# Kernel tuning notes

Hardware: AMD Instinct MI355X
Metric: run time of the kernel (lower is better)

## Reference

```python
import jax, jax.numpy as jnp
import numpy as np

F_DIM = 1024
D = F_DIM // 2          # trunk width (divisor=2)
T = 1024                # contextlen
B = 32
PI = 256
VF = 256
N_HEADS = 4
EPS = 1e-5


def _posenc(seq_len, d):
    pos = jnp.arange(seq_len, dtype=jnp.float32)[:, None]
    div = jnp.exp(jnp.arange(0, d, 2, dtype=jnp.float32) * (-np.log(10000.0) / d))
    pe = jnp.zeros((seq_len, d), dtype=jnp.float32)
    pe = pe.at[:, 0::2].set(jnp.sin(pos * div))
    pe = pe.at[:, 1::2].set(jnp.cos(pos * div))
    return pe


def _ln(x, g, b):
    mu = x.mean(-1, keepdims=True)
    var = ((x - mu) ** 2).mean(-1, keepdims=True)
    return (x - mu) / jnp.sqrt(var + EPS) * g + b


def setup_inputs() -> dict:
    key = jax.random.key(0)
    ks = iter(jax.random.split(key, 40))
    w = lambda shape: jax.random.normal(next(ks), shape, dtype=jnp.float32) * 0.02
    inp = {
        "features": jax.random.normal(next(ks), (B, T, F_DIM), dtype=jnp.float32),
        "enc_w1": w((F_DIM, D)), "enc_b1": jnp.zeros((D,), jnp.float32),
        "enc_w2": w((D, D)),     "enc_b2": jnp.zeros((D,), jnp.float32),
        "qkv_w": w((D, 3 * D)),  "qkv_b": jnp.zeros((3 * D,), jnp.float32),
        "lam": jnp.float32(0.8),
        "out_w": w((D, D)),      "out_b": jnp.zeros((D,), jnp.float32),
        "ln1_g": jnp.ones((D,), jnp.float32), "ln1_b": jnp.zeros((D,), jnp.float32),
        "ffn_w1": w((D, F_DIM)), "ffn_b1": jnp.zeros((F_DIM,), jnp.float32),
        "ffn_w2": w((F_DIM, D)), "ffn_b2": jnp.zeros((D,), jnp.float32),
        "ln2_g": jnp.ones((D,), jnp.float32), "ln2_b": jnp.zeros((D,), jnp.float32),
        "act_w1": w((D, F_DIM)),       "act_b1": jnp.zeros((F_DIM,), jnp.float32),
        "act_w2": w((F_DIM, 2 * F_DIM)), "act_b2": jnp.zeros((2 * F_DIM,), jnp.float32),
        "act_w3": w((2 * F_DIM, PI)),  "act_b3": jnp.zeros((PI,), jnp.float32),
        "cr_w1": w((D, F_DIM)),        "cr_b1": jnp.zeros((F_DIM,), jnp.float32),
        "cr_w2": w((F_DIM, 2 * F_DIM)), "cr_b2": jnp.zeros((2 * F_DIM,), jnp.float32),
        "cr_w3": w((2 * F_DIM, VF)),   "cr_b3": jnp.zeros((VF,), jnp.float32),
    }
    return inp


def reference(features, enc_w1, enc_b1, enc_w2, enc_b2, qkv_w, qkv_b, lam,
              out_w, out_b, ln1_g, ln1_b, ffn_w1, ffn_b1, ffn_w2, ffn_b2,
              ln2_g, ln2_b, act_w1, act_b1, act_w2, act_b2, act_w3, act_b3,
              cr_w1, cr_b1, cr_w2, cr_b2, cr_w3, cr_b3):
    b, t, f = features.shape
    # encoder MLP: feature_dim -> d -> d with ReLU
    y = jax.nn.relu(features @ enc_w1 + enc_b1)
    y = jax.nn.relu(y @ enc_w2 + enc_b2)            # (B,T,D)
    d = y.shape[-1]
    y = y + _posenc(t, d)
    # differential dual-softmax attention (no head split; head_dim only scales)
    qkv = y @ qkv_w + qkv_b
    q, k, v = jnp.split(qkv, 3, axis=-1)
    q1, q2 = jnp.split(q, 2, axis=-1)
    k1, k2 = jnp.split(k, 2, axis=-1)
    scale = 1.0 / np.sqrt(d // N_HEADS)
    a1 = jax.nn.softmax(jnp.einsum('btc,bsc->bts', q1, k1) * scale, axis=-1)
    a2 = jax.nn.softmax(jnp.einsum('btc,bsc->bts', q2, k2) * scale, axis=-1)
    diff = a1 - lam * a2
    attn = jnp.einsum('bts,bsd->btd', diff, v)      # (B,T,D)
    # faithful to torch: transpose(0,1).contiguous().view(B,-1,D)
    attn = jnp.swapaxes(attn, 0, 1).reshape(b, t, d)
    attn = attn @ out_w + out_b
    y = _ln(y + attn, ln1_g, ln1_b)
    z = jax.nn.relu(y @ ffn_w1 + ffn_b1) @ ffn_w2 + ffn_b2
    y = _ln(y + z, ln2_g, ln2_b)                     # (B,T,D)
    # actor / critic heads, then take last timestep
    a = jax.nn.relu(y @ act_w1 + act_b1)
    a = jax.nn.relu(a @ act_w2 + act_b2)
    a = a @ act_w3 + act_b3
    c = jax.nn.relu(y @ cr_w1 + cr_b1)
    c = jax.nn.relu(c @ cr_w2 + cr_b2)
    c = c @ cr_w3 + cr_b3
    return (a[:, -1, :], c[:, -1, :])
```

## Files before the change

### kernel.cpp

```cpp
#include <hip/hip_runtime.h>
#include <hip/hip_bf16.h>
#include <math.h>

#define TDIM 1024
#define FDIM 1024
#define DDIM 512

typedef __attribute__((ext_vector_type(8))) short bf16x8;
typedef __attribute__((ext_vector_type(8))) ushort u16x8;
typedef __attribute__((ext_vector_type(4))) float f32x4;

__device__ __forceinline__ float posenc_val(int t, int c) {
    int j = c >> 1;
    float dv = expf(-9.210340371976184f * (float)(2 * j) * (1.0f / 512.0f));
    float arg = (float)t * dv;
    return (c & 1) ? cosf(arg) : sinf(arg);
}

__device__ __forceinline__ ushort f2bf(float f) {
    __hip_bfloat16 h = __float2bfloat16(f);
    return *reinterpret_cast<ushort*>(&h);
}

template<int BK>
__device__ __forceinline__ void g32_body(
    const float* X, long lda,
    const float* Pin, int KCx, const float* xbias, int xrelu,
    const float* W, long ldb,
    float* Pout, int N, int K,
    int bx, int by, float* lds)
{
    float (*Xs)[BK + 4] = (float (*)[BK + 4])lds;
    float (*Ws)[64]     = (float (*)[64])(lds + 32 * (BK + 4));
    const int tid = threadIdx.x;
    const int n0 = bx * 64, k0 = by * BK;

    {
        const int m  = tid >> 3;
        const int ks = (tid & 7) * (BK / 8);
        if (Pin) {
            #pragma unroll
            for (int j = 0; j < BK / 32; ++j) {
                float4 a = make_float4(0.f, 0.f, 0.f, 0.f);
                for (int c = 0; c < KCx; ++c) {
                    float4 v = *(const float4*)(Pin + (size_t)(c * 32 + m) * K + k0 + ks + j * 4);
                    a.x += v.x; a.y += v.y; a.z += v.z; a.w += v.w;
                }
                if (xbias) {
                    float4 bv = *(const float4*)(xbias + k0 + ks + j * 4);
                    a.x += bv.x; a.y += bv.y; a.z += bv.z; a.w += bv.w;
                }
                if (xrelu) {
                    a.x = fmaxf(a.x, 0.f); a.y = fmaxf(a.y, 0.f);
                    a.z = fmaxf(a.z, 0.f); a.w = fmaxf(a.w, 0.f);
                }
                *(float4*)&Xs[m][ks + j * 4] = a;
            }
        } else {
            const float* src = X + (size_t)m * lda + k0 + ks;
            #pragma unroll
            for (int j = 0; j < BK / 32; ++j)
                *(float4*)&Xs[m][ks + j * 4] = *(const float4*)(src + j * 4);
        }
    }
    #pragma unroll
    for (int it = 0; it < BK / 16; ++it) {
        int e4  = it * 256 + tid;
        int row = e4 >> 4;
        int c4  = e4 & 15;
        *(float4*)&Ws[row][c4 * 4] = *(const float4*)(W + (size_t)(k0 + row) * ldb + n0 + c4 * 4);
    }
    __syncthreads();

    const int tx = tid & 31;
    const int ty = tid >> 5;
    float acc[4][2] = {};
    #pragma unroll 8
    for (int k = 0; k < BK; k += 4) {
        float4 xv[4];
        #pragma unroll
        for (int i = 0; i < 4; ++i) xv[i] = *(const float4*)&Xs[ty * 4 + i][k];
        #pragma unroll
        for (int j = 0; j < 4; ++j) {
            float2 w = *(const float2*)&Ws[k + j][tx * 2];
            #pragma unroll
            for (int i = 0; i < 4; ++i) {
                float x = ((const float*)&xv[i])[j];
                acc[i][0] = fmaf(x, w.x, acc[i][0]);
                acc[i][1] = fmaf(x, w.y, acc[i][1]);
            }
        }
    }
    float* dst = Pout + (size_t)by * 32 * N;
    #pragma unroll
    for (int i = 0; i < 4; ++i)
        *(float2*)(dst + (size_t)(ty * 4 + i) * N + n0 + tx * 2) = make_float2(acc[i][0], acc[i][1]);
}

template<int BK>
__global__ __launch_bounds__(256) void g32k(
    const float* X0, const float* X1, long lda,
    const float* Pin0, const float* Pin1, int KCx,
    const float* xb0, const float* xb1, int xrelu,
    const float* W0, const float* W1, long ldb,
    float* Pout, int N, int K)
{
    __shared__ __align__(16) float lds[32 * (BK + 4) + BK * 64];
    const int z = blockIdx.z;
    g32_body<BK>(z ? X1 : X0, lda, z ? Pin1 : Pin0, KCx, z ? xb1 : xb0, xrelu,
                 z ? W1 : W0, ldb,
                 Pout + (size_t)z * gridDim.y * 32 * N,
                 N, K, blockIdx.x, blockIdx.y, lds);
}

__device__ __forceinline__ void convT_body(const float* W, int ldw, int col0,
                                           ushort* Wt, int K, int bx, int by, float* lds)
{
    float (*t)[33] = (float (*)[33])lds;
    const int k0 = by * 32, n0 = bx * 32;
    const int x = threadIdx.x & 31, y = threadIdx.x >> 5;
    #pragma unroll
    for (int yy = y; yy < 32; yy += 8)
        t[yy][x] = W[(size_t)(k0 + yy) * ldw + col0 + n0 + x];
    __syncthreads();
    #pragma unroll
    for (int yy = y; yy < 32; yy += 8)
        Wt[(size_t)(n0 + yy) * K + k0 + x] = f2bf(t[x][yy]);
}

__device__ __forceinline__ void mfma_body(
    const void* Aptr, int af32, long lda,
    const ushort* Bt, const float* bias,
    float* C, int ldc, ushort* Cbf, int ldcb,
    int K, int relu, int addpe,
    int bx, int by, char* smem)
{
    ushort* Al = (ushort*)smem;
    ushort* Bl = Al + 64 * 64;
    const int tid = threadIdx.x;
    const int m0 = by * 64;
    const int n0 = bx * 64;
    const int lane = tid & 63;
    const int wv = tid >> 6;
    const int wr = wv >> 1, wc = wv & 1;
    const int fr = lane & 15, g = lane >> 4;

    f32x4 acc[2][2] = {};

    const int r0 = tid >> 3;
    const int c0 = tid & 7;

    for (int k0 = 0; k0 < K; k0 += 64) {
        #pragma unroll
        for (int it = 0; it < 2; ++it) {
            int r = r0 + it * 32;
            if (af32) {
                const float* Af = (const float*)Aptr;
                const float* s = Af + (size_t)(m0 + r) * lda + k0 + c0 * 8;
                float4 u = *(const float4*)s;
                float4 v = *(const float4*)(s + 4);
                u16x8 pv;
                pv[0] = f2bf(u.x); pv[1] = f2bf(u.y); pv[2] = f2bf(u.z); pv[3] = f2bf(u.w);
                pv[4] = f2bf(v.x); pv[5] = f2bf(v.y); pv[6] = f2bf(v.z); pv[7] = f2bf(v.w);
                *(u16x8*)((char*)Al + r * 128 + ((c0 ^ (r & 7)) << 4)) = pv;
            } else {
                const ushort* Au = (const ushort*)Aptr;
                uint4 va = *(const uint4*)(Au + (size_t)(m0 + r) * lda + k0 + c0 * 8);
                *(uint4*)((char*)Al + r * 128 + ((c0 ^ (r & 7)) << 4)) = va;
            }
            uint4 vb = *(const uint4*)(Bt + (size_t)(n0 + r) * K + k0 + c0 * 8);
            *(uint4*)((char*)Bl + r * 128 + ((c0 ^ (r & 7)) << 4)) = vb;
        }
        __syncthreads();
        #pragma unroll
        for (int h = 0; h < 2; ++h) {
            bf16x8 af[2], bff[2];
            #pragma unroll
            for (int i = 0; i < 2; ++i) {
                int row = wr * 32 + i * 16 + fr;
                af[i] = *(const bf16x8*)((const char*)Al + row * 128 + (((h * 4 + g) ^ (row & 7)) << 4));
                int col = wc * 32 + i * 16 + fr;
                bff[i] = *(const bf16x8*)((const char*)Bl + col * 128 + (((h * 4 + g) ^ (col & 7)) << 4));
            }
            #pragma unroll
            for (int i = 0; i < 2; ++i)
                #pragma unroll
                for (int j = 0; j < 2; ++j)
                    acc[i][j] = __builtin_amdgcn_mfma_f32_16x16x32_bf16(af[i], bff[j], acc[i][j], 0, 0, 0);
        }
        __syncthreads();
    }

    #pragma unroll
    for (int j = 0; j < 2; ++j) {
        int n = n0 + wc * 32 + j * 16 + fr;
        float bv = bias ? bias[n] : 0.f;
        #pragma unroll
        for (int i = 0; i < 2; ++i) {
            #pragma unroll
            for (int q = 0; q < 4; ++q) {
                int m = m0 + wr * 32 + i * 16 + g * 4 + q;
                float v = acc[i][j][q] + bv;
                if (relu) v = fmaxf(v, 0.f);
                if (addpe) v += posenc_val(m, n);
                if (C)   C[(size_t)m * ldc + n] = v;
                if (Cbf) Cbf[(size_t)m * ldcb + n] = f2bf(v);
            }
        }
    }
}

__global__ __launch_bounds__(256) void mfma_k(
    const void* A, int af32, long lda, const ushort* Bt, const float* bias,
    float* C, int ldc, ushort* Cbf, int ldcb, int K, int relu, int pe)
{
    __shared__ __align__(16) char smem[16384];
    mfma_body(A, af32, lda, Bt, bias, C, ldc, Cbf, ldcb, K, relu, pe,
              blockIdx.x, blockIdx.y, smem);
}

__global__ __launch_bounds__(256) void prep_k(
    const float* features, const float* enc_w1, const float* qkv_w, const float* enc_w2,
    ushort* w1T, ushort* w2T, ushort* qkvT, float* P_enc1)
{
    __shared__ __align__(16) float lds[6272];
    int t = blockIdx.x;
    if (t < 128) {
        g32_body<64>(features + (size_t)1023 * FDIM, (long)TDIM * FDIM,
                     nullptr, 0, nullptr, 0,
                     enc_w1, DDIM, P_enc1, 512, 1024, t & 7, t >> 3, lds);
    } else if (t < 640) {
        int u = t - 128;
        convT_body(enc_w1, 512, 0, w1T, 1024, u & 15, u >> 4, lds);
    } else if (t < 896) {
        int u = t - 640;
        convT_body(enc_w2, 512, 0, w2T, 512, u & 15, u >> 4, lds);
    } else {
        int u = t - 896;
        convT_body(qkv_w, 1536, 0, qkvT, 512, u % 48, u / 48, lds);
    }
}

__global__ __launch_bounds__(256) void stage2_k(
    const float* features31, const ushort* w1T, const float* enc_b1, ushort* H1bf,
    const float* P_enc1, const float* enc_w2, float* P_enc2)
{
    __shared__ __align__(16) char smem[25600];
    int t = blockIdx.x;
    if (t < 128) {
        mfma_body(features31, 1, 1024, w1T, enc_b1, nullptr, 0, H1bf, 512,
                  1024, 1, 0, t & 7, t >> 3, smem);
    } else {
        int u = t - 128;
        g32_body<64>(nullptr, 0, P_enc1, 16, enc_b1, 1,
                     enc_w2, 512, P_enc2, 512, 512, u & 7, u >> 3, (float*)smem);
    }
}

__device__ void scores_body(const float* QKV, float* Psc, int bxs, int byc, char* smem)
{
    float (*Kt)[132] = (float (*)[132])smem;
    float (*Qt)[133] = (float (*)[133])(smem + 64 * 132 * 4);
    const int tid = threadIdx.x;
    const int s0 = bxs * 64;
    const int k0 = byc * 128;

    #pragma unroll
    for (int it = 0; it < 8; ++it) {
        int e4 = it * 256 + tid;
        int r  = e4 >> 5;
        int c4 = e4 & 31;
        float4 v = *(const float4*)(QKV + (size_t)(s0 + r) * 1536 + 512 + k0 + c4 * 4);
        *(float4*)&Kt[r][c4 * 4] = v;
    }
    #pragma unroll
    for (int it = 0; it < 4; ++it) {
        int e4 = it * 256 + tid;
        int r  = e4 >> 5;
        int c4 = e4 & 31;
        float4 v = *(const float4*)(QKV + (size_t)(32 * r + 31) * 1536 + k0 + c4 * 4);
        Qt[r][c4 * 4 + 0] = v.x;
        Qt[r][c4 * 4 + 1] = v.y;
        Qt[r][c4 * 4 + 2] = v.z;
        Qt[r][c4 * 4 + 3] = v.w;
    }
    __syncthreads();

    const int i  = tid & 31;
    const int sg = tid >> 5;
    float acc[8] = {};
    for (int k = 0; k < 128; ++k) {
        float q = Qt[i][k];
        #pragma unroll
        for (int j = 0; j < 8; ++j)
            acc[j] = fmaf(Kt[sg * 8 + j][k], q, acc[j]);
    }
    float* dst = Psc + (size_t)byc * 1024 * 32;
    #pragma unroll
    for (int j = 0; j < 8; ++j)
        dst[(size_t)(s0 + sg * 8 + j) * 32 + i] = acc[j];
}

__global__ __launch_bounds__(256) void stage5_k(
    const float* QKV, float* Psc,
    const float* P_enc2, const float* enc_b2, float* ylast)
{
    __shared__ __align__(16) char smem[50816];
    int t = blockIdx.x;
    if (t < 64) {
        scores_body(QKV, Psc, t & 15, t >> 4, smem);
    } else {
        int blk = t - 64;
        for (int idx = threadIdx.x; idx < 4 * 512; idx += 256) {
            int r = idx >> 9, c = idx & 511;
            int m = blk * 4 + r;
            float s = enc_b2[c];
            for (int cc = 0; cc < 8; ++cc) s += P_enc2[(size_t)(cc * 32 + m) * 512 + c];
            s = fmaxf(s, 0.f) + posenc_val(1023, c);
            ylast[m * 512 + c] = s;
        }
    }
}

__global__ __launch_bounds__(256) void softmax_diff(
    const float* __restrict__ Psc, const float* __restrict__ lam_p, float* __restrict__ D)
{
    __shared__ float sc1[TDIM];
    __shared__ float sc2[TDIM];
    __shared__ float red[256];
    const int i = blockIdx.x;
    const int tid = threadIdx.x;
    const float scale = 0.08838834764831845f;
    for (int s = tid; s < TDIM; s += 256) {
        float a = Psc[(size_t)(0 * 1024 + s) * 32 + i] + Psc[(size_t)(1 * 1024 + s) * 32 + i];
        float b = Psc[(size_t)(2 * 1024 + s) * 32 + i] + Psc[(size_t)(3 * 1024 + s) * 32 + i];
        sc1[s] = a * scale;
        sc2[s] = b * scale;
    }
    __syncthreads();
    float m1 = -INFINITY, m2 = -INFINITY;
    for (int s = tid; s < TDIM; s += 256) { m1 = fmaxf(m1, sc1[s]); m2 = fmaxf(m2, sc2[s]); }
    red[tid] = m1; __syncthreads();
    for (int o = 128; o > 0; o >>= 1) { if (tid < o) red[tid] = fmaxf(red[tid], red[tid + o]); __syncthreads(); }
    m1 = red[0]; __syncthreads();
    red[tid] = m2; __syncthreads();
    for (int o = 128; o > 0; o >>= 1) { if (tid < o) red[tid] = fmaxf(red[tid], red[tid + o]); __syncthreads(); }
    m2 = red[0]; __syncthreads();
    float t1 = 0.f, t2 = 0.f;
    for (int s = tid; s < TDIM; s += 256) { t1 += expf(sc1[s] - m1); t2 += expf(sc2[s] - m2); }
    red[tid] = t1; __syncthreads();
    for (int o = 128; o > 0; o >>= 1) { if (tid < o) red[tid] += red[tid + o]; __syncthreads(); }
    t1 = red[0]; __syncthreads();
    red[tid] = t2; __syncthreads();
    for (int o = 128; o > 0; o >>= 1) { if (tid < o) red[tid] += red[tid + o]; __syncthreads(); }
    t2 = red[0]; __syncthreads();
    const float inv1 = 1.f / t1, inv2 = 1.f / t2;
    const float lam = *lam_p;
    for (int s = tid; s < TDIM; s += 256)
        D[(size_t)i * TDIM + s] = expf(sc1[s] - m1) * inv1 - lam * expf(sc2[s] - m2) * inv2;
}

__global__ __launch_bounds__(256) void ln_red(
    const float* __restrict__ Pin, int KC, const float* __restrict__ bias,
    const float* __restrict__ R, const float* __restrict__ g, const float* __restrict__ b,
    float* __restrict__ Y)
{
    __shared__ float red[256];
    const int m = blockIdx.x;
    const int tid = threadIdx.x;
    float v0 = bias ? bias[tid] : 0.f;
    float v1 = bias ? bias[tid + 256] : 0.f;
    for (int c = 0; c < KC; ++c) {
        v0 += Pin[(size_t)(c * 32 + m) * 512 + tid];
        v1 += Pin[(size_t)(c * 32 + m) * 512 + tid + 256];
    }
    v0 += R[m * 512 + tid];
    v1 += R[m * 512 + tid + 256];
    red[tid] = v0 + v1; __syncthreads();
    for (int o = 128; o > 0; o >>= 1) { if (tid < o) red[tid] += red[tid + o]; __syncthreads(); }
    const float mu = red[0] * (1.0f / 512.0f);
    __syncthreads();
    float d0 = v0 - mu, d1 = v1 - mu;
    red[tid] = d0 * d0 + d1 * d1; __syncthreads();
    for (int o = 128; o > 0; o >>= 1) { if (tid < o) red[tid] += red[tid + o]; __syncthreads(); }
    const float var = red[0] * (1.0f / 512.0f);
    const float inv = 1.0f / sqrtf(var + 1e-5f);
    Y[m * 512 + tid]       = d0 * inv * g[tid]       + b[tid];
    Y[m * 512 + 256 + tid] = d1 * inv * g[256 + tid] + b[256 + tid];
}

__global__ __launch_bounds__(256) void fin_out(
    const float* __restrict__ P, const float* __restrict__ b0, const float* __restrict__ b1,
    float* __restrict__ out)
{
    const int m = blockIdx.x;
    const int z = blockIdx.y;
    const int n = threadIdx.x;
    const float* bias = z ? b1 : b0;
    const float* Pz = P + (size_t)z * 16 * 32 * 256;
    float s = bias[n];
    for (int c = 0; c < 16; ++c) s += Pz[(size_t)(c * 32 + m) * 256 + n];
    out[z * 8192 + m * 256 + n] = s;
}

extern "C" void kernel_launch(void* const* d_in, const int* in_sizes, int n_in,
                              void* d_out, int out_size, void* d_ws, size_t ws_size,
                              hipStream_t stream)
{
    const float* features = (const float*)d_in[0];
    const float* enc_w1 = (const float*)d_in[1];
    const float* enc_b1 = (const float*)d_in[2];
    const float* enc_w2 = (const float*)d_in[3];
    const float* enc_b2 = (const float*)d_in[4];
    const float* qkv_w  = (const float*)d_in[5];
    const float* qkv_b  = (const float*)d_in[6];
    const float* lam    = (const float*)d_in[7];
    const float* out_w  = (const float*)d_in[8];
    const float* out_b  = (const float*)d_in[9];
    const float* ln1_g  = (const float*)d_in[10];
    const float* ln1_b  = (const float*)d_in[11];
    const float* ffn_w1 = (const float*)d_in[12];
    const float* ffn_b1 = (const float*)d_in[13];
    const float* ffn_w2 = (const float*)d_in[14];
    const float* ffn_b2 = (const float*)d_in[15];
    const float* ln2_g  = (const float*)d_in[16];
    const float* ln2_b  = (const float*)d_in[17];
    const float* act_w1 = (const float*)d_in[18];
    const float* act_b1 = (const float*)d_in[19];
    const float* act_w2 = (const float*)d_in[20];
    const float* act_b2 = (const float*)d_in[21];
    const float* act_w3 = (const float*)d_in[22];
    const float* act_b3 = (const float*)d_in[23];
    const float* cr_w1  = (const float*)d_in[24];
    const float* cr_b1  = (const float*)d_in[25];
    const float* cr_w2  = (const float*)d_in[26];
    const float* cr_b2  = (const float*)d_in[27];
    const float* cr_w3  = (const float*)d_in[28];
    const float* cr_b3  = (const float*)d_in[29];
    float* out = (float*)d_out;

    char* base = (char*)d_ws;
    ushort* w1T    = (ushort*)(base + 0x000000);
    ushort* w2T    = (ushort*)(base + 0x100000);
    ushort* qkvT   = (ushort*)(base + 0x180000);
    ushort* H1bf   = (ushort*)(base + 0x300000);
    ushort* Y31bf  = (ushort*)(base + 0x400000);
    float*  QKV    = (float*)(base + 0x500000);
    float*  Psc    = (float*)(base + 0xB00000);
    float*  Dbuf   = (float*)(base + 0xB80000);
    float*  ylast  = (float*)(base + 0xBA0000);
    float*  y1     = (float*)(base + 0xBB0000);
    float*  y2     = (float*)(base + 0xBC0000);
    float*  P_enc1 = (float*)(base + 0xC00000);
    float*  P_enc2 = (float*)(base + 0xD00000);
    float*  P_attn = (float*)(base + 0xD80000);
    float*  P_atp  = (float*)(base + 0xE80000);
    float*  P_h    = (float*)(base + 0xF00000);
    float*  P_z    = (float*)(base + 0x1000000);
    float*  P_a1   = (float*)(base + 0x1100000);
    float*  P_a2   = (float*)(base + 0x1300000);
    float*  P_a3   = (float*)(base + 0x1700000);

    const float* features31 = features + (size_t)31 * TDIM * FDIM;
    dim3 blk(256);
    const float* NPF = nullptr;

    prep_k<<<1664, blk, 0, stream>>>(features, enc_w1, qkv_w, enc_w2, w1T, w2T, qkvT, P_enc1);
    stage2_k<<<192, blk, 0, stream>>>(features31, w1T, enc_b1, H1bf, P_enc1, enc_w2, P_enc2);
    mfma_k<<<dim3(8, 16), blk, 0, stream>>>(H1bf, 0, 512, w2T, enc_b2,
                                            nullptr, 0, Y31bf, 512, 512, 1, 1);
    mfma_k<<<dim3(24, 16), blk, 0, stream>>>(Y31bf, 0, 512, qkvT, qkv_b,
                                             QKV, 1536, nullptr, 0, 512, 0, 0);
    stage5_k<<<72, blk, 0, stream>>>(QKV, Psc, P_enc2, enc_b2, ylast);
    softmax_diff<<<32, blk, 0, stream>>>(Psc, lam, Dbuf);
    g32k<64><<<dim3(8, 16, 1), blk, 0, stream>>>(Dbuf, NPF, 1024, NPF, NPF, 0, NPF, NPF, 0,
                                                 QKV + 1024, NPF, 1536, P_attn, 512, 1024);
    g32k<64><<<dim3(8, 8, 1), blk, 0, stream>>>(NPF, NPF, 0, P_attn, NPF, 16, NPF, NPF, 0,
                                                out_w, NPF, 512, P_atp, 512, 512);
    ln_red<<<32, blk, 0, stream>>>(P_atp, 8, out_b, ylast, ln1_g, ln1_b, y1);
    g32k<64><<<dim3(16, 8, 1), blk, 0, stream>>>(y1, NPF, 512, NPF, NPF, 0, NPF, NPF, 0,
                                                 ffn_w1, NPF, 1024, P_h, 1024, 512);
    g32k<64><<<dim3(8, 16, 1), blk, 0, stream>>>(NPF, NPF, 0, P_h, NPF, 8, ffn_b1, NPF, 1,
                                                 ffn_w2, NPF, 512, P_z, 512, 1024);
    ln_red<<<32, blk, 0, stream>>>(P_z, 16, ffn_b2, y1, ln2_g, ln2_b, y2);
    g32k<64><<<dim3(16, 8, 2), blk, 0, stream>>>(y2, y2, 512, NPF, NPF, 0, NPF, NPF, 0,
                                                 act_w1, cr_w1, 1024, P_a1, 1024, 512);
    g32k<128><<<dim3(32, 8, 2), blk, 0, stream>>>(NPF, NPF, 0, P_a1, P_a1 + 8 * 32 * 1024, 8,
                                                  act_b1, cr_b1, 1,
                                                  act_w2, cr_w2, 2048, P_a2, 2048, 1024);
    g32k<128><<<dim3(4, 16, 2), blk, 0, stream>>>(NPF, NPF, 0, P_a2, P_a2 + 8 * 32 * 2048, 8,
                                                  act_b2, cr_b2, 1,
                                                  act_w3, cr_w3, 256, P_a3, 256, 2048);
    fin_out<<<dim3(32, 2), blk, 0, stream>>>(P_a3, act_b3, cr_b3, out);
}
```

Measured before the change: 141.6 us.

## Fuse LayerNorm into following GEMMs, compute Q only for needed rows, rebalance split-K

Replaces the separate LayerNorm reduction kernels with a fused kernel that computes the row statistics and normalises the rows while staging the next GEMM's input. The Q projection now runs only on the 32 rows that are used, with K/V kept in a separate buffer. The stage-3 matmul is merged with the ylast reduction into one launch. The split-K GEMMs move to larger BK, with an optional multi-stage K loop that shrinks the partial-sum fan-in. The intent is fewer launches and less redundant work, at the cost of recomputing LN statistics in every block and of lower parallelism in some GEMMs.

```diff
diff --git a/kernel.cpp b/kernel.cpp
--- a/kernel.cpp
+++ b/kernel.cpp
@@ -22,7 +22,7 @@
     return *reinterpret_cast<ushort*>(&h);
 }
 
-template<int BK>
+template<int BK, int NS>
 __device__ __forceinline__ void g32_body(
     const float* X, long lda,
     const float* Pin, int KCx, const float* xbias, int xrelu,
@@ -33,63 +33,68 @@
     float (*Xs)[BK + 4] = (float (*)[BK + 4])lds;
     float (*Ws)[64]     = (float (*)[64])(lds + 32 * (BK + 4));
     const int tid = threadIdx.x;
-    const int n0 = bx * 64, k0 = by * BK;
-
-    {
-        const int m  = tid >> 3;
-        const int ks = (tid & 7) * (BK / 8);
-        if (Pin) {
-            #pragma unroll
-            for (int j = 0; j < BK / 32; ++j) {
-                float4 a = make_float4(0.f, 0.f, 0.f, 0.f);
-                for (int c = 0; c < KCx; ++c) {
-                    float4 v = *(const float4*)(Pin + (size_t)(c * 32 + m) * K + k0 + ks + j * 4);
-                    a.x += v.x; a.y += v.y; a.z += v.z; a.w += v.w;
-                }
-                if (xbias) {
-                    float4 bv = *(const float4*)(xbias + k0 + ks + j * 4);
-                    a.x += bv.x; a.y += bv.y; a.z += bv.z; a.w += bv.w;
-                }
-                if (xrelu) {
-                    a.x = fmaxf(a.x, 0.f); a.y = fmaxf(a.y, 0.f);
-                    a.z = fmaxf(a.z, 0.f); a.w = fmaxf(a.w, 0.f);
-                }
-                *(float4*)&Xs[m][ks + j * 4] = a;
-            }
-        } else {
-            const float* src = X + (size_t)m * lda + k0 + ks;
-            #pragma unroll
-            for (int j = 0; j < BK / 32; ++j)
-                *(float4*)&Xs[m][ks + j * 4] = *(const float4*)(src + j * 4);
-        }
-    }
-    #pragma unroll
-    for (int it = 0; it < BK / 16; ++it) {
-        int e4  = it * 256 + tid;
-        int row = e4 >> 4;
-        int c4  = e4 & 15;
-        *(float4*)&Ws[row][c4 * 4] = *(const float4*)(W + (size_t)(k0 + row) * ldb + n0 + c4 * 4);
-    }
-    __syncthreads();
+    const int n0 = bx * 64;
 
     const int tx = tid & 31;
     const int ty = tid >> 5;
     float acc[4][2] = {};
-    #pragma unroll 8
-    for (int k = 0; k < BK; k += 4) {
-        float4 xv[4];
-        #pragma unroll
-        for (int i = 0; i < 4; ++i) xv[i] = *(const float4*)&Xs[ty * 4 + i][k];
-        #pragma unroll
-        for (int j = 0; j < 4; ++j) {
-            float2 w = *(const float2*)&Ws[k + j][tx * 2];
+
+    for (int st = 0; st < NS; ++st) {
+        const int k0 = (by * NS + st) * BK;
+        {
+            const int m  = tid >> 3;
+            const int ks = (tid & 7) * (BK / 8);
+            if (Pin) {
+                #pragma unroll
+                for (int j = 0; j < BK / 32; ++j) {
+                    float4 a = make_float4(0.f, 0.f, 0.f, 0.f);
+                    for (int c = 0; c < KCx; ++c) {
+                        float4 v = *(const float4*)(Pin + (size_t)(c * 32 + m) * K + k0 + ks + j * 4);
+                        a.x += v.x; a.y += v.y; a.z += v.z; a.w += v.w;
+                    }
+                    if (xbias) {
+                        float4 bv = *(const float4*)(xbias + k0 + ks + j * 4);
+                        a.x += bv.x; a.y += bv.y; a.z += bv.z; a.w += bv.w;
+                    }
+                    if (xrelu) {
+                        a.x = fmaxf(a.x, 0.f); a.y = fmaxf(a.y, 0.f);
+                        a.z = fmaxf(a.z, 0.f); a.w = fmaxf(a.w, 0.f);
+                    }
+                    *(float4*)&Xs[m][ks + j * 4] = a;
+                }
+            } else {
+                const float* src = X + (size_t)m * lda + k0 + ks;
+                #pragma unroll
+                for (int j = 0; j < BK / 32; ++j)
+                    *(float4*)&Xs[m][ks + j * 4] = *(const float4*)(src + j * 4);
+            }
+        }
+        #pragma unroll
+        for (int it = 0; it < BK / 16; ++it) {
+            int e4  = it * 256 + tid;
+            int row = e4 >> 4;
+            int c4  = e4 & 15;
+            *(float4*)&Ws[row][c4 * 4] = *(const float4*)(W + (size_t)(k0 + row) * ldb + n0 + c4 * 4);
+        }
+        __syncthreads();
+
+        #pragma unroll 8
+        for (int k = 0; k < BK; k += 4) {
+            float4 xv[4];
             #pragma unroll
-            for (int i = 0; i < 4; ++i) {
-                float x = ((const float*)&xv[i])[j];
-                acc[i][0] = fmaf(x, w.x, acc[i][0]);
-                acc[i][1] = fmaf(x, w.y, acc[i][1]);
-            }
-        }
+            for (int i = 0; i < 4; ++i) xv[i] = *(const float4*)&Xs[ty * 4 + i][k];
+            #pragma unroll
+            for (int j = 0; j < 4; ++j) {
+                float2 w = *(const float2*)&Ws[k + j][tx * 2];
+                #pragma unroll
+                for (int i = 0; i < 4; ++i) {
+                    float x = ((const float*)&xv[i])[j];
+                    acc[i][0] = fmaf(x, w.x, acc[i][0]);
+                    acc[i][1] = fmaf(x, w.y, acc[i][1]);
+                }
+            }
+        }
+        __syncthreads();
     }
     float* dst = Pout + (size_t)by * 32 * N;
     #pragma unroll
@@ -97,7 +102,7 @@
         *(float2*)(dst + (size_t)(ty * 4 + i) * N + n0 + tx * 2) = make_float2(acc[i][0], acc[i][1]);
 }
 
-template<int BK>
+template<int BK, int NS>
 __global__ __launch_bounds__(256) void g32k(
     const float* X0, const float* X1, long lda,
     const float* Pin0, const float* Pin1, int KCx,
@@ -107,10 +112,10 @@
 {
     __shared__ __align__(16) float lds[32 * (BK + 4) + BK * 64];
     const int z = blockIdx.z;
-    g32_body<BK>(z ? X1 : X0, lda, z ? Pin1 : Pin0, KCx, z ? xb1 : xb0, xrelu,
-                 z ? W1 : W0, ldb,
-                 Pout + (size_t)z * gridDim.y * 32 * N,
-                 N, K, blockIdx.x, blockIdx.y, lds);
+    g32_body<BK, NS>(z ? X1 : X0, lda, z ? Pin1 : Pin0, KCx, z ? xb1 : xb0, xrelu,
+                     z ? W1 : W0, ldb,
+                     Pout + (size_t)z * gridDim.y * 32 * N,
+                     N, K, blockIdx.x, blockIdx.y, lds);
 }
 
 __device__ __forceinline__ void convT_body(const float* W, int ldw, int col0,
@@ -133,7 +138,7 @@
     const ushort* Bt, const float* bias,
     float* C, int ldc, ushort* Cbf, int ldcb,
     int K, int relu, int addpe,
-    int bx, int by, char* smem)
+    int bx, int by, char* smem, int rowmap, int mvalid)
 {
     ushort* Al = (ushort*)smem;
     ushort* Bl = Al + 64 * 64;
@@ -154,9 +159,10 @@
         #pragma unroll
         for (int it = 0; it < 2; ++it) {
             int r = r0 + it * 32;
+            int ar = rowmap ? (31 + 32 * (r < 32 ? r : 31)) : (m0 + r);
             if (af32) {
                 const float* Af = (const float*)Aptr;
-                const float* s = Af + (size_t)(m0 + r) * lda + k0 + c0 * 8;
+                const float* s = Af + (size_t)ar * lda + k0 + c0 * 8;
                 float4 u = *(const float4*)s;
                 float4 v = *(const float4*)(s + 4);
                 u16x8 pv;
@@ -165,7 +171,7 @@
                 *(u16x8*)((char*)Al + r * 128 + ((c0 ^ (r & 7)) << 4)) = pv;
             } else {
                 const ushort* Au = (const ushort*)Aptr;
-                uint4 va = *(const uint4*)(Au + (size_t)(m0 + r) * lda + k0 + c0 * 8);
+                uint4 va = *(const uint4*)(Au + (size_t)ar * lda + k0 + c0 * 8);
                 *(uint4*)((char*)Al + r * 128 + ((c0 ^ (r & 7)) << 4)) = va;
             }
             uint4 vb = *(const uint4*)(Bt + (size_t)(n0 + r) * K + k0 + c0 * 8);
@@ -200,6 +206,7 @@
             #pragma unroll
             for (int q = 0; q < 4; ++q) {
                 int m = m0 + wr * 32 + i * 16 + g * 4 + q;
+                if (m >= mvalid) continue;
                 float v = acc[i][j][q] + bv;
                 if (relu) v = fmaxf(v, 0.f);
                 if (addpe) v += posenc_val(m, n);
@@ -210,15 +217,6 @@
     }
 }
 
-__global__ __launch_bounds__(256) void mfma_k(
-    const void* A, int af32, long lda, const ushort* Bt, const float* bias,
-    float* C, int ldc, ushort* Cbf, int ldcb, int K, int relu, int pe)
-{
-    __shared__ __align__(16) char smem[16384];
-    mfma_body(A, af32, lda, Bt, bias, C, ldc, Cbf, ldcb, K, relu, pe,
-              blockIdx.x, blockIdx.y, smem);
-}
-
 __global__ __launch_bounds__(256) void prep_k(
     const float* features, const float* enc_w1, const float* qkv_w, const float* enc_w2,
     ushort* w1T, ushort* w2T, ushort* qkvT, float* P_enc1)
@@ -226,18 +224,15 @@
     __shared__ __align__(16) float lds[6272];
     int t = blockIdx.x;
     if (t < 128) {
-        g32_body<64>(features + (size_t)1023 * FDIM, (long)TDIM * FDIM,
-                     nullptr, 0, nullptr, 0,
-                     enc_w1, DDIM, P_enc1, 512, 1024, t & 7, t >> 3, lds);
+        g32_body<64, 1>(features + (size_t)1023 * FDIM, (long)TDIM * FDIM,
+                        nullptr, 0, nullptr, 0,
+                        enc_w1, DDIM, P_enc1, 512, 1024, t & 7, t >> 3, lds);
     } else if (t < 640) {
-        int u = t - 128;
-        convT_body(enc_w1, 512, 0, w1T, 1024, u & 15, u >> 4, lds);
+        int u = t - 128; convT_body(enc_w1, 512, 0, w1T, 1024, u & 15, u >> 4, lds);
     } else if (t < 896) {
-        int u = t - 640;
-        convT_body(enc_w2, 512, 0, w2T, 512, u & 15, u >> 4, lds);
+        int u = t - 640; convT_body(enc_w2, 512, 0, w2T, 512, u & 15, u >> 4, lds);
     } else {
-        int u = t - 896;
-        convT_body(qkv_w, 1536, 0, qkvT, 512, u % 48, u / 48, lds);
+        int u = t - 896; convT_body(qkv_w, 1536, 0, qkvT, 512, u % 48, u / 48, lds);
     }
 }
 
@@ -245,32 +240,70 @@
     const float* features31, const ushort* w1T, const float* enc_b1, ushort* H1bf,
     const float* P_enc1, const float* enc_w2, float* P_enc2)
 {
-    __shared__ __align__(16) char smem[25600];
+    __shared__ __align__(16) char smem[51200];
     int t = blockIdx.x;
     if (t < 128) {
         mfma_body(features31, 1, 1024, w1T, enc_b1, nullptr, 0, H1bf, 512,
-                  1024, 1, 0, t & 7, t >> 3, smem);
+                  1024, 1, 0, t & 7, t >> 3, smem, 0, 1024);
     } else {
-        int u = t - 128;
-        g32_body<64>(nullptr, 0, P_enc1, 16, enc_b1, 1,
-                     enc_w2, 512, P_enc2, 512, 512, u & 7, u >> 3, (float*)smem);
-    }
-}
-
-__device__ void scores_body(const float* QKV, float* Psc, int bxs, int byc, char* smem)
-{
-    float (*Kt)[132] = (float (*)[132])smem;
-    float (*Qt)[133] = (float (*)[133])(smem + 64 * 132 * 4);
+        int v = t - 128;
+        g32_body<64, 1>(nullptr, 0, P_enc1, 16, enc_b1, 1,
+                        enc_w2, 512, P_enc2, 512, 512, v & 7, v >> 3, (float*)smem);
+    }
+}
+
+__global__ __launch_bounds__(256) void stage3_k(
+    const ushort* H1bf, const ushort* w2T, const float* enc_b2, ushort* Y31bf,
+    const float* P_enc2, float* ylast)
+{
+    __shared__ __align__(16) char smem[16384];
+    int t = blockIdx.x;
+    if (t < 128) {
+        mfma_body(H1bf, 0, 512, w2T, enc_b2, nullptr, 0, Y31bf, 512,
+                  512, 1, 1, t & 7, t >> 3, smem, 0, 1024);
+    } else {
+        int m = t - 128;
+        #pragma unroll
+        for (int half = 0; half < 2; ++half) {
+            int c = threadIdx.x + half * 256;
+            float s = enc_b2[c];
+            for (int cc = 0; cc < 8; ++cc) s += P_enc2[(size_t)(cc * 32 + m) * 512 + c];
+            s = fmaxf(s, 0.f) + posenc_val(1023, c);
+            ylast[m * 512 + c] = s;
+        }
+    }
+}
+
+__global__ __launch_bounds__(256) void stage4_k(
+    const ushort* Y31bf, const ushort* qkvT, const float* qkv_b,
+    float* KV, float* Q32)
+{
+    __shared__ __align__(16) char smem[16384];
+    int u = blockIdx.x;
+    if (u < 256) {
+        mfma_body(Y31bf, 0, 512, qkvT + (size_t)512 * 512, qkv_b + 512,
+                  KV, 1024, nullptr, 0, 512, 0, 0, u & 15, u >> 4, smem, 0, 1024);
+    } else {
+        mfma_body(Y31bf, 0, 512, qkvT, qkv_b,
+                  Q32, 512, nullptr, 0, 512, 0, 0, u - 256, 0, smem, 1, 32);
+    }
+}
+
+__global__ __launch_bounds__(256) void scores_kernel(
+    const float* __restrict__ KV, const float* __restrict__ Q32, float* __restrict__ Psc)
+{
+    __shared__ float Kt[64][132];
+    __shared__ float Qt[32][133];
     const int tid = threadIdx.x;
-    const int s0 = bxs * 64;
-    const int k0 = byc * 128;
+    const int s0 = blockIdx.x * 64;
+    const int k0 = blockIdx.y * 128;
 
     #pragma unroll
     for (int it = 0; it < 8; ++it) {
         int e4 = it * 256 + tid;
         int r  = e4 >> 5;
         int c4 = e4 & 31;
-        float4 v = *(const float4*)(QKV + (size_t)(s0 + r) * 1536 + 512 + k0 + c4 * 4);
+        float4 v = *(const float4*)(KV + (size_t)(s0 + r) * 1024 + k0 + c4 * 4);
         *(float4*)&Kt[r][c4 * 4] = v;
     }
     #pragma unroll
@@ -278,7 +311,7 @@
         int e4 = it * 256 + tid;
         int r  = e4 >> 5;
         int c4 = e4 & 31;
-        float4 v = *(const float4*)(QKV + (size_t)(32 * r + 31) * 1536 + k0 + c4 * 4);
+        float4 v = *(const float4*)(Q32 + (size_t)r * 512 + k0 + c4 * 4);
         Qt[r][c4 * 4 + 0] = v.x;
         Qt[r][c4 * 4 + 1] = v.y;
         Qt[r][c4 * 4 + 2] = v.z;
@@ -295,31 +328,10 @@
         for (int j = 0; j < 8; ++j)
             acc[j] = fmaf(Kt[sg * 8 + j][k], q, acc[j]);
     }
-    float* dst = Psc + (size_t)byc * 1024 * 32;
+    float* dst = Psc + (size_t)blockIdx.y * 1024 * 32;
     #pragma unroll
     for (int j = 0; j < 8; ++j)
         dst[(size_t)(s0 + sg * 8 + j) * 32 + i] = acc[j];
-}
-
-__global__ __launch_bounds__(256) void stage5_k(
-    const float* QKV, float* Psc,
-    const float* P_enc2, const float* enc_b2, float* ylast)
-{
-    __shared__ __align__(16) char smem[50816];
-    int t = blockIdx.x;
-    if (t < 64) {
-        scores_body(QKV, Psc, t & 15, t >> 4, smem);
-    } else {
-        int blk = t - 64;
-        for (int idx = threadIdx.x; idx < 4 * 512; idx += 256) {
-            int r = idx >> 9, c = idx & 511;
-            int m = blk * 4 + r;
-            float s = enc_b2[c];
-            for (int cc = 0; cc < 8; ++cc) s += P_enc2[(size_t)(cc * 32 + m) * 512 + c];
-            s = fmaxf(s, 0.f) + posenc_val(1023, c);
-            ylast[m * 512 + c] = s;
-        }
-    }
 }
 
 __global__ __launch_bounds__(256) void softmax_diff(
@@ -332,8 +344,8 @@
     const int tid = threadIdx.x;
     const float scale = 0.08838834764831845f;
     for (int s = tid; s < TDIM; s += 256) {
-        float a = Psc[(size_t)(0 * 1024 + s) * 32 + i] + Psc[(size_t)(1 * 1024 + s) * 32 + i];
-        float b = Psc[(size_t)(2 * 1024 + s) * 32 + i] + Psc[(size_t)(3 * 1024 + s) * 32 + i];
+        float a = Psc[(size_t)s * 32 + i] + Psc[(size_t)(1024 + s) * 32 + i];
+        float b = Psc[(size_t)(2048 + s) * 32 + i] + Psc[(size_t)(3072 + s) * 32 + i];
         sc1[s] = a * scale;
         sc2[s] = b * scale;
     }
@@ -360,33 +372,104 @@
         D[(size_t)i * TDIM + s] = expf(sc1[s] - m1) * inv1 - lam * expf(sc2[s] - m2) * inv2;
 }
 
-__global__ __launch_bounds__(256) void ln_red(
-    const float* __restrict__ Pin, int KC, const float* __restrict__ bias,
-    const float* __restrict__ R, const float* __restrict__ g, const float* __restrict__ b,
-    float* __restrict__ Y)
-{
-    __shared__ float red[256];
-    const int m = blockIdx.x;
+__global__ __launch_bounds__(256) void lngemm_k(
+    const float* __restrict__ Pin, int KC,
+    const float* __restrict__ inb, const float* __restrict__ R,
+    const float* __restrict__ g, const float* __restrict__ b,
+    const float* __restrict__ W0, const float* __restrict__ W1, int ldw,
+    float* __restrict__ Pout, int N, float* __restrict__ Yout)
+{
+    __shared__ float Xs[32][68];
+    __shared__ float Ws[64][64];
+    __shared__ float st1[32][8];
+    __shared__ float st2[32][8];
+    __shared__ float mu_s[32], inv_s[32];
     const int tid = threadIdx.x;
-    float v0 = bias ? bias[tid] : 0.f;
-    float v1 = bias ? bias[tid + 256] : 0.f;
-    for (int c = 0; c < KC; ++c) {
-        v0 += Pin[(size_t)(c * 32 + m) * 512 + tid];
-        v1 += Pin[(size_t)(c * 32 + m) * 512 + tid + 256];
-    }
-    v0 += R[m * 512 + tid];
-    v1 += R[m * 512 + tid + 256];
-    red[tid] = v0 + v1; __syncthreads();
-    for (int o = 128; o > 0; o >>= 1) { if (tid < o) red[tid] += red[tid + o]; __syncthreads(); }
-    const float mu = red[0] * (1.0f / 512.0f);
+    const int n0 = blockIdx.x * 64, k0 = blockIdx.y * 64;
+    const float* W = blockIdx.z ? W1 : W0;
+
+    {
+        const int i = tid >> 3, p = tid & 7;
+        float s1 = 0.f, s2 = 0.f;
+        for (int q4 = 0; q4 < 16; ++q4) {
+            int n = p * 64 + q4 * 4;
+            float4 v = *(const float4*)(inb + n);
+            float4 r = *(const float4*)(R + i * 512 + n);
+            v.x += r.x; v.y += r.y; v.z += r.z; v.w += r.w;
+            for (int c = 0; c < KC; ++c) {
+                float4 pv = *(const float4*)(Pin + (size_t)(c * 32 + i) * 512 + n);
+                v.x += pv.x; v.y += pv.y; v.z += pv.z; v.w += pv.w;
+            }
+            s1 += v.x + v.y + v.z + v.w;
+            s2 += v.x * v.x + v.y * v.y + v.z * v.z + v.w * v.w;
+        }
+        st1[i][p] = s1; st2[i][p] = s2;
+    }
     __syncthreads();
-    float d0 = v0 - mu, d1 = v1 - mu;
-    red[tid] = d0 * d0 + d1 * d1; __syncthreads();
-    for (int o = 128; o > 0; o >>= 1) { if (tid < o) red[tid] += red[tid + o]; __syncthreads(); }
-    const float var = red[0] * (1.0f / 512.0f);
-    const float inv = 1.0f / sqrtf(var + 1e-5f);
-    Y[m * 512 + tid]       = d0 * inv * g[tid]       + b[tid];
-    Y[m * 512 + 256 + tid] = d1 * inv * g[256 + tid] + b[256 + tid];
+    if (tid < 32) {
+        float s1 = 0.f, s2 = 0.f;
+        #pragma unroll
+        for (int p = 0; p < 8; ++p) { s1 += st1[tid][p]; s2 += st2[tid][p]; }
+        float mu = s1 * (1.0f / 512.0f);
+        float var = s2 * (1.0f / 512.0f) - mu * mu;
+        mu_s[tid] = mu;
+        inv_s[tid] = 1.0f / sqrtf(var + 1e-5f);
+    }
+    #pragma unroll
+    for (int it = 0; it < 4; ++it) {
+        int e4 = it * 256 + tid;
+        int row = e4 >> 4, c4 = e4 & 15;
+        *(float4*)&Ws[row][c4 * 4] = *(const float4*)(W + (size_t)(k0 + row) * ldw + n0 + c4 * 4);
+    }
+    __syncthreads();
+    {
+        const int m = tid >> 3, f = tid & 7;
+        float mu = mu_s[m], iv = inv_s[m];
+        #pragma unroll
+        for (int h = 0; h < 2; ++h) {
+            int n = k0 + f * 8 + h * 4;
+            float4 v = *(const float4*)(inb + n);
+            float4 r = *(const float4*)(R + m * 512 + n);
+            v.x += r.x; v.y += r.y; v.z += r.z; v.w += r.w;
+            for (int c = 0; c < KC; ++c) {
+                float4 pv = *(const float4*)(Pin + (size_t)(c * 32 + m) * 512 + n);
+                v.x += pv.x; v.y += pv.y; v.z += pv.z; v.w += pv.w;
+            }
+            float4 gg = *(const float4*)(g + n);
+            float4 bb = *(const float4*)(b + n);
+            float4 y;
+            y.x = (v.x - mu) * iv * gg.x + bb.x;
+            y.y = (v.y - mu) * iv * gg.y + bb.y;
+            y.z = (v.z - mu) * iv * gg.z + bb.z;
+            y.w = (v.w - mu) * iv * gg.w + bb.w;
+            *(float4*)&Xs[m][f * 8 + h * 4] = y;
+            if (Yout && blockIdx.x == 0)
+                *(float4*)(Yout + m * 512 + n) = y;
+        }
+    }
+    __syncthreads();
+    const int tx = tid & 31, ty = tid >> 5;
+    float acc[4][2] = {};
+    #pragma unroll 8
+    for (int k = 0; k < 64; k += 4) {
+        float4 xv[4];
+        #pragma unroll
+        for (int i = 0; i < 4; ++i) xv[i] = *(const float4*)&Xs[ty * 4 + i][k];
+        #pragma unroll
+        for (int j = 0; j < 4; ++j) {
+            float2 w = *(const float2*)&Ws[k + j][tx * 2];
+            #pragma unroll
+            for (int i = 0; i < 4; ++i) {
+                float x = ((const float*)&xv[i])[j];
+                acc[i][0] = fmaf(x, w.x, acc[i][0]);
+                acc[i][1] = fmaf(x, w.y, acc[i][1]);
+            }
+        }
+    }
+    float* dst = Pout + (size_t)(blockIdx.z * gridDim.y + blockIdx.y) * 32 * N;
+    #pragma unroll
+    for (int i = 0; i < 4; ++i)
+        *(float2*)(dst + (size_t)(ty * 4 + i) * N + n0 + tx * 2) = make_float2(acc[i][0], acc[i][1]);
 }
 
 __global__ __launch_bounds__(256) void fin_out(
@@ -440,26 +523,26 @@
     float* out = (float*)d_out;
 
     char* base = (char*)d_ws;
-    ushort* w1T    = (ushort*)(base + 0x000000);
-    ushort* w2T    = (ushort*)(base + 0x100000);
-    ushort* qkvT   = (ushort*)(base + 0x180000);
-    ushort* H1bf   = (ushort*)(base + 0x300000);
-    ushort* Y31bf  = (ushort*)(base + 0x400000);
-    float*  QKV    = (float*)(base + 0x500000);
-    float*  Psc    = (float*)(base + 0xB00000);
-    float*  Dbuf   = (float*)(base + 0xB80000);
-    float*  ylast  = (float*)(base + 0xBA0000);
-    float*  y1     = (float*)(base + 0xBB0000);
-    float*  y2     = (float*)(base + 0xBC0000);
-    float*  P_enc1 = (float*)(base + 0xC00000);
-    float*  P_enc2 = (float*)(base + 0xD00000);
-    float*  P_attn = (float*)(base + 0xD80000);
+    float*  KV     = (float*)(base + 0x000000);
+    float*  Q32    = (float*)(base + 0x400000);
+    float*  P_enc1 = (float*)(base + 0x420000);
+    float*  P_enc2 = (float*)(base + 0x520000);
+    float*  ylast  = (float*)(base + 0x5A0000);
+    float*  y1     = (float*)(base + 0x5B0000);
+    ushort* w1T    = (ushort*)(base + 0x600000);
+    ushort* w2T    = (ushort*)(base + 0x700000);
+    ushort* qkvT   = (ushort*)(base + 0x780000);
+    ushort* H1bf   = (ushort*)(base + 0x900000);
+    ushort* Y31bf  = (ushort*)(base + 0xA00000);
+    float*  Psc    = (float*)(base + 0xD00000);
+    float*  Dbuf   = (float*)(base + 0xD80000);
+    float*  P_attn = (float*)(base + 0xE00000);
     float*  P_atp  = (float*)(base + 0xE80000);
     float*  P_h    = (float*)(base + 0xF00000);
     float*  P_z    = (float*)(base + 0x1000000);
-    float*  P_a1   = (float*)(base + 0x1100000);
-    float*  P_a2   = (float*)(base + 0x1300000);
-    float*  P_a3   = (float*)(base + 0x1700000);
+    float*  P_a1   = (float*)(base + 0x000000);
+    float*  P_a2   = (float*)(base + 0x600000);
+    float*  P_a3   = (float*)(base + 0xA00000);
 
     const float* features31 = features + (size_t)31 * TDIM * FDIM;
     dim3 blk(256);
@@ -467,29 +550,25 @@
 
     prep_k<<<1664, blk, 0, stream>>>(features, enc_w1, qkv_w, enc_w2, w1T, w2T, qkvT, P_enc1);
     stage2_k<<<192, blk, 0, stream>>>(features31, w1T, enc_b1, H1bf, P_enc1, enc_w2, P_enc2);
-    mfma_k<<<dim3(8, 16), blk, 0, stream>>>(H1bf, 0, 512, w2T, enc_b2,
-                                            nullptr, 0, Y31bf, 512, 512, 1, 1);
-    mfma_k<<<dim3(24, 16), blk, 0, stream>>>(Y31bf, 0, 512, qkvT, qkv_b,
-                                             QKV, 1536, nullptr, 0, 512, 0, 0);
-    stage5_k<<<72, blk, 0, stream>>>(QKV, Psc, P_enc2, enc_b2, ylast);
+    stage3_k<<<160, blk, 0, stream>>>(H1bf, w2T, enc_b2, Y31bf, P_enc2, ylast);
+    stage4_k<<<264, blk, 0, stream>>>(Y31bf, qkvT, qkv_b, KV, Q32);
+    scores_kernel<<<dim3(16, 4), blk, 0, stream>>>(KV, Q32, Psc);
     softmax_diff<<<32, blk, 0, stream>>>(Psc, lam, Dbuf);
-    g32k<64><<<dim3(8, 16, 1), blk, 0, stream>>>(Dbuf, NPF, 1024, NPF, NPF, 0, NPF, NPF, 0,
-                                                 QKV + 1024, NPF, 1536, P_attn, 512, 1024);
-    g32k<64><<<dim3(8, 8, 1), blk, 0, stream>>>(NPF, NPF, 0, P_attn, NPF, 16, NPF, NPF, 0,
-                                                out_w, NPF, 512, P_atp, 512, 512);
-    ln_red<<<32, blk, 0, stream>>>(P_atp, 8, out_b, ylast, ln1_g, ln1_b, y1);
-    g32k<64><<<dim3(16, 8, 1), blk, 0, stream>>>(y1, NPF, 512, NPF, NPF, 0, NPF, NPF, 0,
-                                                 ffn_w1, NPF, 1024, P_h, 1024, 512);
-    g32k<64><<<dim3(8, 16, 1), blk, 0, stream>>>(NPF, NPF, 0, P_h, NPF, 8, ffn_b1, NPF, 1,
-                                                 ffn_w2, NPF, 512, P_z, 512, 1024);
-    ln_red<<<32, blk, 0, stream>>>(P_z, 16, ffn_b2, y1, ln2_g, ln2_b, y2);
-    g32k<64><<<dim3(16, 8, 2), blk, 0, stream>>>(y2, y2, 512, NPF, NPF, 0, NPF, NPF, 0,
-                                                 act_w1, cr_w1, 1024, P_a1, 1024, 512);
-    g32k<128><<<dim3(32, 8, 2), blk, 0, stream>>>(NPF, NPF, 0, P_a1, P_a1 + 8 * 32 * 1024, 8,
-                                                  act_b1, cr_b1, 1,
-                                                  act_w2, cr_w2, 2048, P_a2, 2048, 1024);
-    g32k<128><<<dim3(4, 16, 2), blk, 0, stream>>>(NPF, NPF, 0, P_a2, P_a2 + 8 * 32 * 2048, 8,
-                                                  act_b2, cr_b2, 1,
-                                                  act_w3, cr_w3, 256, P_a3, 256, 2048);
+    g32k<128, 1><<<dim3(8, 8, 1), blk, 0, stream>>>(Dbuf, NPF, 1024, NPF, NPF, 0, NPF, NPF, 0,
+                                                    KV + 512, NPF, 1024, P_attn, 512, 1024);
+    g32k<128, 1><<<dim3(8, 4, 1), blk, 0, stream>>>(NPF, NPF, 0, P_attn, NPF, 8, NPF, NPF, 0,
+                                                    out_w, NPF, 512, P_atp, 512, 512);
+    lngemm_k<<<dim3(16, 8, 1), blk, 0, stream>>>(P_atp, 4, out_b, ylast, ln1_g, ln1_b,
+                                                 ffn_w1, NPF, 1024, P_h, 1024, y1);
+    g32k<128, 2><<<dim3(8, 4, 1), blk, 0, stream>>>(NPF, NPF, 0, P_h, NPF, 8, ffn_b1, NPF, 1,
+                                                    ffn_w2, NPF, 512, P_z, 512, 1024);
+    lngemm_k<<<dim3(16, 8, 2), blk, 0, stream>>>(P_z, 4, ffn_b2, y1, ln2_g, ln2_b,
+                                                 act_w1, cr_w1, 1024, P_a1, 1024, (float*)nullptr);
+    g32k<128, 1><<<dim3(32, 8, 2), blk, 0, stream>>>(NPF, NPF, 0, P_a1, P_a1 + (size_t)8 * 32 * 1024, 8,
+                                                     act_b1, cr_b1, 1,
+                                                     act_w2, cr_w2, 2048, P_a2, 2048, 1024);
+    g32k<128, 1><<<dim3(4, 16, 2), blk, 0, stream>>>(NPF, NPF, 0, P_a2, P_a2 + (size_t)8 * 32 * 2048, 8,
+                                                     act_b2, cr_b2, 1,
+                                                     act_w3, cr_w3, 256, P_a3, 256, 2048);
     fin_out<<<dim3(32, 2), blk, 0, stream>>>(P_a3, act_b3, cr_b3, out);
 }
```

After: 192.1 us. 1.36x slower.
